# Performance work log

Measured on AMD Instinct MI355X. Metric: run time of the kernel, lower is better.

The kernel has to match this reference:

```python
import jax, jax.numpy as jnp
import numpy as np

B, S, E, D, L, H = 8, 1024, 512, 1024, 8, 16
HD = D // H                 # 64
ROT = max(HD // 2, 32)      # 32
FF = 4 * D
FUSED = 3 * D + 2 * FF      # q,k,v,ff,ff_gate
EPS = 1e-5


def layer_norm(x, w, b):
    mu = jnp.mean(x, axis=-1, keepdims=True)
    var = jnp.mean(jnp.square(x - mu), axis=-1, keepdims=True)
    return (x - mu) * jax.lax.rsqrt(var + EPS) * w + b


def gelu(x):  # fused_gelu from source (erf form, constant 1.41421)
    return x * 0.5 * (1.0 + jax.scipy.special.erf(x / 1.41421))


def silu(x):
    return x * jax.nn.sigmoid(x)


def rotate_half(x):
    x1, x2 = jnp.split(x, 2, axis=-1)
    return jnp.concatenate([-x2, x1], axis=-1)


def rope_tables(seq_len):
    inv = 1.0 / (10000.0 ** (jnp.arange(0, ROT, 2, dtype=jnp.float32) / ROT))
    freqs = jnp.arange(seq_len, dtype=jnp.float32)[:, None] * inv[None, :]
    emb = jnp.concatenate([freqs, freqs], axis=-1)  # [S, ROT]
    # source caches sin/cos in bfloat16 (precision=torch.bfloat16)
    sin = jnp.sin(emb).astype(jnp.bfloat16).astype(jnp.float32)[None, None]
    cos = jnp.cos(emb).astype(jnp.bfloat16).astype(jnp.float32)[None, None]
    return sin, cos  # [1,1,S,ROT]


def setup_inputs() -> dict:
    key = jax.random.key(0)
    ks = jax.random.split(key, 24)
    std = 0.02
    inp = {
        "noisy_embeds": jax.random.normal(ks[0], (B, S, E), jnp.float32),
        "cond_embeds": jax.random.normal(ks[1], (B, S, E), jnp.float32),
        "prev_embeds": jax.random.normal(ks[2], (B, S, E), jnp.float32),
        "infill_mask": jax.random.uniform(ks[3], (B, S, 1), jnp.float32),
        "attention_mask": jnp.zeros((B, 1, 1, S), jnp.float32),
        "times": jax.random.uniform(ks[4], (B,), jnp.float32),
        # time embedding params
        "fourier_w": jax.random.normal(ks[5], (D // 2, 1), jnp.float32),
        "t1_w": jax.random.normal(ks[6], (D, D), jnp.float32) * std,
        "t1_b": jnp.zeros((D,), jnp.float32),
        "t2_w": jax.random.normal(ks[7], (D, D), jnp.float32) * std,
        "t2_b": jnp.zeros((D,), jnp.float32),
        # input projection
        "in_w": jax.random.normal(ks[8], (D, 4 * E), jnp.float32) * std,
        "in_b": jnp.zeros((D,), jnp.float32),
        # per-layer (stacked) block params
        "ln_w": jnp.ones((L, D), jnp.float32),
        "ln_b": jnp.zeros((L, D), jnp.float32),
        "cond_w": jax.random.normal(ks[9], (L, 2 * D, D), jnp.float32) * std,
        "cond_b": jnp.zeros((L, 2 * D), jnp.float32),
        "proj_w": jax.random.normal(ks[10], (L, FUSED, D), jnp.float32) * std,
        "attn_w": jax.random.normal(ks[11], (L, D, D), jnp.float32) * std,
        "attn_b": jnp.zeros((L, D), jnp.float32),
        "ff_w": jax.random.normal(ks[12], (L, D, FF), jnp.float32) * std,
        "ff_b": jnp.zeros((L, D), jnp.float32),
        # output head
        "outln_w": jnp.ones((D,), jnp.float32),
        "outln_b": jnp.zeros((D,), jnp.float32),
        "out_w": jax.random.normal(ks[13], (E, D), jnp.float32) * std,
        "out_b": jnp.zeros((E,), jnp.float32),
        "fin_w": jnp.ones((E,), jnp.float32),
        "fin_b": jnp.zeros((E,), jnp.float32),
    }
    return inp


def _split_heads(x):  # [B,S,H*hd] -> [B,H,S,hd]
    return x.reshape(B, S, H, HD).transpose(0, 2, 1, 3)


def _forward(noisy_embeds, cond_embeds, prev_embeds, infill_mask, attention_mask,
             times, fourier_w, t1_w, t1_b, t2_w, t2_b, in_w, in_b,
             ln_w, ln_b, cond_w, cond_b, proj_w, attn_w, attn_b, ff_w, ff_b,
             outln_w, outln_b, out_w, out_b, fin_w, fin_b):
    # -- time embedding (Random Fourier + MLP) --
    f = 2.0 * np.pi * (times[:, None] @ fourier_w.T)          # [B, D/2]
    te = jnp.concatenate([jnp.cos(f), jnp.sin(f)], axis=-1)   # [B, D]
    te = gelu(te @ t1_w.T + t1_b) @ t2_w.T + t2_b             # [B, D]
    time_embeds = te[:, None, :]                              # [B, 1, D]

    # -- input projection: cat(noisy, cond, prev, mask broadcast) --
    mask_feat = infill_mask * jnp.ones_like(noisy_embeds)     # [B,S,E]
    x = jnp.concatenate([noisy_embeds, cond_embeds, prev_embeds, mask_feat], axis=-1)
    h = x @ in_w.T + in_b                                     # [B,S,D]

    sin, cos = rope_tables(S)
    sm_scale = HD ** (-0.5)

    for i in range(L):
        units = layer_norm(h, ln_w[i], ln_b[i])
        # FiLM conditioning
        sb = silu(time_embeds) @ cond_w[i].T + cond_b[i]      # [B,1,2D]
        scale, bias = jnp.split(sb, 2, axis=-1)
        units = (1.0 + scale) * units + bias
        # fused projection and split
        proj = units @ proj_w[i].T                            # [B,S,11D]
        q, k, v, ff, ff_gate = jnp.split(
            proj, np.cumsum([D, D, D, FF])[:4].tolist(), axis=-1)
        q, k, v = _split_heads(q), _split_heads(k), _split_heads(v)  # [B,H,S,hd]
        # rotary on first ROT dims
        q = jnp.concatenate(
            [q[..., :ROT] * cos + rotate_half(q[..., :ROT]) * sin, q[..., ROT:]], axis=-1)
        k = jnp.concatenate(
            [k[..., :ROT] * cos + rotate_half(k[..., :ROT]) * sin, k[..., ROT:]], axis=-1)
        # NOTE: source scales BOTH q and k by hd^-0.5 (effective hd^-1)
        score = jnp.einsum('bhsd,bhSd->bhsS', q * sm_scale, k * sm_scale)
        score = score + attention_mask
        w = jax.nn.softmax(score, axis=-1)
        attn = jnp.einsum('bhsS,bhSd->bhsd', w, v)
        merged = attn.transpose(0, 2, 1, 3).reshape(B, S, D)
        attn_out = merged @ attn_w[i].T + attn_b[i]
        ff_out = (ff * gelu(ff_gate)) @ ff_w[i].T + ff_b[i]
        h = h + attn_out + ff_out

    out = layer_norm(h, outln_w, outln_b) @ out_w.T + out_b   # [B,S,E]
    return layer_norm(out, fin_w, fin_b)


def reference(noisy_embeds, cond_embeds, prev_embeds, infill_mask, attention_mask,
              times, fourier_w, t1_w, t1_b, t2_w, t2_b, in_w, in_b,
              ln_w, ln_b, cond_w, cond_b, proj_w, attn_w, attn_b, ff_w, ff_b,
              outln_w, outln_b, out_w, out_b, fin_w, fin_b):
    return _forward(noisy_embeds, cond_embeds, prev_embeds, infill_mask, attention_mask,
                    times, fourier_w, t1_w, t1_b, t2_w, t2_b, in_w, in_b,
                    ln_w, ln_b, cond_w, cond_b, proj_w, attn_w, attn_b, ff_w, ff_b,
                    outln_w, outln_b, out_w, out_b, fin_w, fin_b)
```

## Files before the change

kernel.cpp:

```cpp
#include <hip/hip_runtime.h>
#include <hip/hip_bf16.h>
#include <cstddef>
#include <cstdint>

#define BB 8
#define SS 1024
#define EE 512
#define DD 1024
#define LL 8
#define HH 16
#define HD 64
#define ROT 32
#define FF 4096
#define FUSED 11264
#define NTOK 8192
#define QKVW 3072

using u16 = unsigned short;
typedef __attribute__((ext_vector_type(8))) __bf16 bf16x8;
typedef __attribute__((ext_vector_type(4))) float f32x4;
typedef __attribute__((ext_vector_type(4))) unsigned short u16x4;
typedef __attribute__((ext_vector_type(8))) unsigned short u16x8;

typedef const __attribute__((address_space(1))) void gas_t;
typedef __attribute__((address_space(3))) void las_t;

__device__ __forceinline__ void gld16(const void* g, void* l) {
  __builtin_amdgcn_global_load_lds((gas_t*)g, (las_t*)l, 16, 0, 0);
}

__device__ __forceinline__ float bf2f(u16 u) {
  union { unsigned int i; float f; } v; v.i = ((unsigned int)u) << 16; return v.f;
}
__device__ __forceinline__ u16 f2bf(float f) {
  union { float f; unsigned int i; } v; v.f = f;
  unsigned int u = v.i;
  unsigned int r = u + 0x7FFFu + ((u >> 16) & 1u);
  return (u16)(r >> 16);
}
__device__ __forceinline__ float gelu_f(float x) {
  return x * 0.5f * (1.0f + erff(x / 1.41421f));
}
__device__ __forceinline__ float silu_f(float x) {
  return x / (1.0f + __expf(-x));
}

template <int ACCUM, int OUTBF16>
__global__ __launch_bounds__(256, 2) void gemm_bt(
    const u16* __restrict__ A, const u16* __restrict__ W,
    const float* __restrict__ bias, void* __restrict__ Cp,
    int M, int N, int K) {
  __shared__ __align__(16) u16 As[2][128 * 64];
  __shared__ __align__(16) u16 Bs[2][128 * 64];
  const int tid = threadIdx.x;
  const int w = tid >> 6, lane = tid & 63;
  const int m0 = blockIdx.y * 128, n0 = blockIdx.x * 128;
  const int wm = w >> 1, wn = w & 1;

  f32x4 acc[4][4] = {};

  auto stage = [&](int buf, int k0) {
#pragma unroll
    for (int i = 0; i < 4; i++) {
      const int c = w + i * 4;
      const int r = c * 8 + (lane >> 3);
      const int colb = ((lane & 7) << 4) ^ ((r & 7) << 4);
      gld16(A + (size_t)(m0 + r) * K + k0 + (colb >> 1), &As[buf][c * 512]);
      gld16(W + (size_t)(n0 + r) * K + k0 + (colb >> 1), &Bs[buf][c * 512]);
    }
  };

  const int nt = K >> 6;
  stage(0, 0);
  stage(1, 64);
  __syncthreads();

  for (int t = 0; t < nt; t++) {
    const int cur = t & 1;
    bf16x8 av0[4], bv0[4], av1[4], bv1[4];
#pragma unroll
    for (int m = 0; m < 4; m++) {
      const int row = wm * 64 + m * 16 + (lane & 15);
      const int sw = (row & 7) << 4;
      av0[m] = *(const bf16x8*)((const char*)As[cur] + row * 128 + ((((lane >> 4) << 4)) ^ sw));
      av1[m] = *(const bf16x8*)((const char*)As[cur] + row * 128 + ((64 + ((lane >> 4) << 4)) ^ sw));
    }
#pragma unroll
    for (int n = 0; n < 4; n++) {
      const int row = wn * 64 + n * 16 + (lane & 15);
      const int sw = (row & 7) << 4;
      bv0[n] = *(const bf16x8*)((const char*)Bs[cur] + row * 128 + ((((lane >> 4) << 4)) ^ sw));
      bv1[n] = *(const bf16x8*)((const char*)Bs[cur] + row * 128 + ((64 + ((lane >> 4) << 4)) ^ sw));
    }
    __builtin_amdgcn_s_setprio(1);
#pragma unroll
    for (int m = 0; m < 4; m++)
#pragma unroll
      for (int n = 0; n < 4; n++)
        acc[m][n] = __builtin_amdgcn_mfma_f32_16x16x32_bf16(av0[m], bv0[n], acc[m][n], 0, 0, 0);
    __builtin_amdgcn_s_setprio(0);
    __builtin_amdgcn_sched_barrier(0);
    __syncthreads();
    if (t + 2 < nt) stage(cur, (t + 2) << 6);
    __builtin_amdgcn_s_setprio(1);
#pragma unroll
    for (int m = 0; m < 4; m++)
#pragma unroll
      for (int n = 0; n < 4; n++)
        acc[m][n] = __builtin_amdgcn_mfma_f32_16x16x32_bf16(av1[m], bv1[n], acc[m][n], 0, 0, 0);
    __builtin_amdgcn_s_setprio(0);
  }

  const int rowb0 = m0 + wm * 64 + ((lane >> 4) << 2);
  const int colb0 = n0 + wn * 64 + (lane & 15);
#pragma unroll
  for (int n = 0; n < 4; n++) {
    const int col = colb0 + n * 16;
    const float bn = bias ? bias[col] : 0.0f;
#pragma unroll
    for (int m = 0; m < 4; m++) {
#pragma unroll
      for (int r = 0; r < 4; r++) {
        const size_t idx = (size_t)(rowb0 + m * 16 + r) * N + col;
        const float v = acc[m][n][r] + bn;
        if (ACCUM) {
          ((float*)Cp)[idx] += v;
        } else if (OUTBF16) {
          ((u16*)Cp)[idx] = f2bf(v);
        } else {
          ((float*)Cp)[idx] = v;
        }
      }
    }
  }
}

template <int GATED>
__global__ __launch_bounds__(512, 2) void gemm_bt256(
    const u16* __restrict__ A, const u16* __restrict__ W,
    void* __restrict__ Cp, int M, int N, int K) {
  __shared__ __align__(16) u16 As[2][256 * 64];
  __shared__ __align__(16) u16 Bs[2][256 * 64];
  const int tid = threadIdx.x;
  const int w = tid >> 6, lane = tid & 63;
  const int m0 = blockIdx.y * 256, n0 = blockIdx.x * 256;
  const int wm = w >> 2, wn = w & 3;

  f32x4 acc[8][4] = {};

  auto stage = [&](int buf, int k0) {
#pragma unroll
    for (int i = 0; i < 4; i++) {
      const int c = w + i * 8;
      const int r = c * 8 + (lane >> 3);
      const int colb = ((lane & 7) << 4) ^ ((r & 7) << 4);
      gld16(A + (size_t)(m0 + r) * K + k0 + (colb >> 1), &As[buf][c * 512]);
      gld16(W + (size_t)(n0 + r) * K + k0 + (colb >> 1), &Bs[buf][c * 512]);
    }
  };

  const int nt = K >> 6;
  stage(0, 0);
  stage(1, 64);
  __syncthreads();

  for (int t = 0; t < nt; t++) {
    const int cur = t & 1;
    {
      bf16x8 av0[8], bv0[4];
#pragma unroll
      for (int m = 0; m < 8; m++) {
        const int row = wm * 128 + m * 16 + (lane & 15);
        const int cb = (((lane >> 4) << 4)) ^ ((row & 7) << 4);
        av0[m] = *(const bf16x8*)((const char*)As[cur] + row * 128 + cb);
      }
#pragma unroll
      for (int n = 0; n < 4; n++) {
        const int row = wn * 64 + n * 16 + (lane & 15);
        const int cb = (((lane >> 4) << 4)) ^ ((row & 7) << 4);
        bv0[n] = *(const bf16x8*)((const char*)Bs[cur] + row * 128 + cb);
      }
      __builtin_amdgcn_s_setprio(1);
#pragma unroll
      for (int m = 0; m < 8; m++)
#pragma unroll
        for (int n = 0; n < 4; n++)
          acc[m][n] = __builtin_amdgcn_mfma_f32_16x16x32_bf16(av0[m], bv0[n], acc[m][n], 0, 0, 0);
      __builtin_amdgcn_s_setprio(0);
    }
    bf16x8 av1[8], bv1[4];
#pragma unroll
    for (int m = 0; m < 8; m++) {
      const int row = wm * 128 + m * 16 + (lane & 15);
      const int cb = (64 + ((lane >> 4) << 4)) ^ ((row & 7) << 4);
      av1[m] = *(const bf16x8*)((const char*)As[cur] + row * 128 + cb);
    }
#pragma unroll
    for (int n = 0; n < 4; n++) {
      const int row = wn * 64 + n * 16 + (lane & 15);
      const int cb = (64 + ((lane >> 4) << 4)) ^ ((row & 7) << 4);
      bv1[n] = *(const bf16x8*)((const char*)Bs[cur] + row * 128 + cb);
    }
    __builtin_amdgcn_sched_barrier(0);
    __syncthreads();
    if (t + 2 < nt) stage(cur, (t + 2) << 6);
    __builtin_amdgcn_s_setprio(1);
#pragma unroll
    for (int m = 0; m < 8; m++)
#pragma unroll
      for (int n = 0; n < 4; n++)
        acc[m][n] = __builtin_amdgcn_mfma_f32_16x16x32_bf16(av1[m], bv1[n], acc[m][n], 0, 0, 0);
    __builtin_amdgcn_s_setprio(0);
  }

  const int rowb0 = m0 + wm * 128 + ((lane >> 4) << 2);
  if (GATED) {
    const int No = N >> 1;
#pragma unroll
    for (int n = 0; n < 4; n += 2) {
      const int outcol = (n0 >> 1) + wn * 32 + ((n >> 1) << 4) + (lane & 15);
#pragma unroll
      for (int m = 0; m < 8; m++)
#pragma unroll
        for (int r = 0; r < 4; r++) {
          const float fv = acc[m][n][r];
          const float gv = acc[m][n + 1][r];
          ((u16*)Cp)[(size_t)(rowb0 + m * 16 + r) * No + outcol] = f2bf(fv * gelu_f(gv));
        }
    }
  } else {
    const int colb0 = n0 + wn * 64 + (lane & 15);
#pragma unroll
    for (int n = 0; n < 4; n++) {
      const int col = colb0 + n * 16;
#pragma unroll
      for (int m = 0; m < 8; m++)
#pragma unroll
        for (int r = 0; r < 4; r++)
          ((u16*)Cp)[(size_t)(rowb0 + m * 16 + r) * N + col] = f2bf(acc[m][n][r]);
    }
  }
}

__global__ __launch_bounds__(256, 2) void attn_fwd(
    const u16* __restrict__ qr, const u16* __restrict__ kr,
    const u16* __restrict__ vt, const float* __restrict__ mask,
    u16* __restrict__ merged) {
  __shared__ __align__(16) u16 Ks[2][128 * 64];
  __shared__ __align__(16) u16 Vs[2][64 * 128];
  __shared__ __align__(16) u16 Ps[4][16 * 128];
  const int tid = threadIdx.x, w = tid >> 6, lane = tid & 63;
  const int g = blockIdx.x;
  const int j = g >> 3;
  const int bh = (g & 7) + ((j >> 4) << 3);
  const int qx = j & 15;
  const int b = bh >> 4;
  const int q0 = qx * 64 + w * 16;
  const u16* Qb = qr + (size_t)bh * SS * HD;
  const u16* Kb = kr + (size_t)bh * SS * HD;
  const u16* Vb = vt + (size_t)bh * HD * SS;
  const float* mb = mask + (size_t)b * SS;

  bf16x8 qf0, qf1;
  {
    const int qrow = q0 + (lane & 15);
    const u16* qp = Qb + (size_t)qrow * HD + ((lane >> 4) << 3);
    qf0 = *(const bf16x8*)qp;
    qf1 = *(const bf16x8*)(qp + 32);
  }

  float mrun[4], srun[4];
  f32x4 acc[4] = {};
#pragma unroll
  for (int r = 0; r < 4; r++) { mrun[r] = -1e30f; srun[r] = 0.0f; }

  u16* pw = &Ps[w][0];

  auto stage = [&](int buf, int kv0) {
#pragma unroll
    for (int i = 0; i < 4; i++) {
      const int c = w + i * 4;
      {
        const int r = c * 8 + (lane >> 3);
        const int colb = ((lane & 7) << 4) ^ ((r & 7) << 4);
        gld16(Kb + (size_t)(kv0 + r) * HD + (colb >> 1), &Ks[buf][c * 512]);
      }
      {
        const int d = c * 4 + (lane >> 4);
        const int colb = ((lane & 15) << 4) ^ ((d & 7) << 4);
        gld16(Vb + (size_t)d * SS + kv0 + (colb >> 1), &Vs[buf][c * 512]);
      }
    }
  };

  stage(0, 0);
  __syncthreads();

  for (int t = 0; t < 8; t++) {
    const int cur = t & 1;
    const int kv0 = t * 128;
    if (t < 7) stage(cur ^ 1, kv0 + 128);

    f32x4 p[8];
    __builtin_amdgcn_s_setprio(1);
#pragma unroll
    for (int blk = 0; blk < 8; blk++) {
      const int row = blk * 16 + (lane & 15);
      const int swz = (row & 7) << 4;
      const bf16x8 k0v = *(const bf16x8*)((const char*)Ks[cur] + row * 128 + ((((lane >> 4) << 4)) ^ swz));
      const bf16x8 k1v = *(const bf16x8*)((const char*)Ks[cur] + row * 128 + ((64 + ((lane >> 4) << 4)) ^ swz));
      f32x4 z = {};
      p[blk] = __builtin_amdgcn_mfma_f32_16x16x32_bf16(qf0, k0v, z, 0, 0, 0);
      p[blk] = __builtin_amdgcn_mfma_f32_16x16x32_bf16(qf1, k1v, p[blk], 0, 0, 0);
    }
    __builtin_amdgcn_s_setprio(0);

    float mv[8];
#pragma unroll
    for (int blk = 0; blk < 8; blk++) mv[blk] = mb[kv0 + blk * 16 + (lane & 15)];
#pragma unroll
    for (int blk = 0; blk < 8; blk++)
#pragma unroll
      for (int r = 0; r < 4; r++) p[blk][r] = p[blk][r] * (1.0f / 64.0f) + mv[blk];

    float fac[4];
#pragma unroll
    for (int r = 0; r < 4; r++) {
      float tm = p[0][r];
#pragma unroll
      for (int blk = 1; blk < 8; blk++) tm = fmaxf(tm, p[blk][r]);
      tm = fmaxf(tm, __shfl_xor(tm, 1));
      tm = fmaxf(tm, __shfl_xor(tm, 2));
      tm = fmaxf(tm, __shfl_xor(tm, 4));
      tm = fmaxf(tm, __shfl_xor(tm, 8));
      const float mn = fmaxf(mrun[r], tm);
      fac[r] = __expf(mrun[r] - mn);
      mrun[r] = mn;
      float rs = 0.0f;
#pragma unroll
      for (int blk = 0; blk < 8; blk++) {
        const float e = __expf(p[blk][r] - mn);
        p[blk][r] = e;
        rs += e;
      }
      rs += __shfl_xor(rs, 1);
      rs += __shfl_xor(rs, 2);
      rs += __shfl_xor(rs, 4);
      rs += __shfl_xor(rs, 8);
      srun[r] = srun[r] * fac[r] + rs;
    }
#pragma unroll
    for (int dblk = 0; dblk < 4; dblk++)
#pragma unroll
      for (int r = 0; r < 4; r++) acc[dblk][r] *= fac[r];

#pragma unroll
    for (int blk = 0; blk < 8; blk++)
#pragma unroll
      for (int r = 0; r < 4; r++) {
        const int q = ((lane >> 4) << 2) + r;
        pw[(q * 128 + blk * 16 + (lane & 15)) ^ ((q & 7) << 3)] = f2bf(p[blk][r]);
      }

    bf16x8 pa[4];
#pragma unroll
    for (int ks = 0; ks < 4; ks++) {
      const int q = lane & 15;
      pa[ks] = *(const bf16x8*)(pw + ((q * 128 + ks * 32 + ((lane >> 4) << 3)) ^ ((q & 7) << 3)));
    }

    __builtin_amdgcn_s_setprio(1);
#pragma unroll
    for (int dblk = 0; dblk < 4; dblk++) {
      const int drow = dblk * 16 + (lane & 15);
      const int swz = (drow & 7) << 4;
#pragma unroll
      for (int ks = 0; ks < 4; ks++) {
        const bf16x8 vv = *(const bf16x8*)((const char*)Vs[cur] + drow * 256 + ((ks * 64 + ((lane >> 4) << 4)) ^ swz));
        acc[dblk] = __builtin_amdgcn_mfma_f32_16x16x32_bf16(pa[ks], vv, acc[dblk], 0, 0, 0);
      }
    }
    __builtin_amdgcn_s_setprio(0);

    __syncthreads();
  }

#pragma unroll
  for (int dblk = 0; dblk < 4; dblk++)
#pragma unroll
    for (int r = 0; r < 4; r++) {
      const int sq = q0 + ((lane >> 4) << 2) + r;
      const int d = dblk * 16 + (lane & 15);
      merged[((size_t)b * SS + sq) * DD + (bh & 15) * HD + d] = f2bf(acc[dblk][r] / srun[r]);
    }
}

__global__ __launch_bounds__(256) void ln_mod(
    const float* __restrict__ x, const float* __restrict__ lw,
    const float* __restrict__ lb, const float* __restrict__ sb,
    u16* __restrict__ out) {
  const int row = blockIdx.x, tid = threadIdx.x;
  const float4 v = ((const float4*)(x + (size_t)row * DD))[tid];
  float vv[4] = {v.x, v.y, v.z, v.w};
  float s = vv[0] + vv[1] + vv[2] + vv[3];
  float q = vv[0] * vv[0] + vv[1] * vv[1] + vv[2] * vv[2] + vv[3] * vv[3];
  for (int off = 1; off < 64; off <<= 1) {
    s += __shfl_xor(s, off);
    q += __shfl_xor(q, off);
  }
  __shared__ float red[8];
  const int w = tid >> 6, lane = tid & 63;
  if (lane == 0) { red[w] = s; red[4 + w] = q; }
  __syncthreads();
  s = red[0] + red[1] + red[2] + red[3];
  q = red[4] + red[5] + red[6] + red[7];
  const float mu = s * (1.0f / DD);
  const float inv = rsqrtf(q * (1.0f / DD) - mu * mu + 1e-5f);
  const int b = row >> 10;
  u16x4 o;
#pragma unroll
  for (int j = 0; j < 4; j++) {
    const int d = tid * 4 + j;
    float g = (vv[j] - mu) * inv * lw[d] + lb[d];
    if (sb) g = (1.0f + sb[(size_t)b * 2048 + d]) * g + sb[(size_t)b * 2048 + DD + d];
    o[j] = f2bf(g);
  }
  *(u16x4*)(out + (size_t)row * DD + tid * 4) = o;
}

__global__ __launch_bounds__(128) void ln_fin(
    const float* __restrict__ x, const float* __restrict__ w_,
    const float* __restrict__ b_, float* __restrict__ out) {
  const int row = blockIdx.x, tid = threadIdx.x;
  const float4 v = ((const float4*)(x + (size_t)row * EE))[tid];
  float vv[4] = {v.x, v.y, v.z, v.w};
  float s = vv[0] + vv[1] + vv[2] + vv[3];
  float q = vv[0] * vv[0] + vv[1] * vv[1] + vv[2] * vv[2] + vv[3] * vv[3];
  for (int off = 1; off < 64; off <<= 1) {
    s += __shfl_xor(s, off);
    q += __shfl_xor(q, off);
  }
  __shared__ float red[4];
  const int w = tid >> 6, lane = tid & 63;
  if (lane == 0) { red[w] = s; red[2 + w] = q; }
  __syncthreads();
  s = red[0] + red[1];
  q = red[2] + red[3];
  const float mu = s * (1.0f / EE);
  const float inv = rsqrtf(q * (1.0f / EE) - mu * mu + 1e-5f);
  float4 o;
  o.x = (vv[0] - mu) * inv * w_[tid * 4 + 0] + b_[tid * 4 + 0];
  o.y = (vv[1] - mu) * inv * w_[tid * 4 + 1] + b_[tid * 4 + 1];
  o.z = (vv[2] - mu) * inv * w_[tid * 4 + 2] + b_[tid * 4 + 2];
  o.w = (vv[3] - mu) * inv * w_[tid * 4 + 3] + b_[tid * 4 + 3];
  ((float4*)(out + (size_t)row * EE))[tid] = o;
}

template <int IA, int OA>
__global__ __launch_bounds__(256) void vec_gemm(
    const float* __restrict__ in, const float* __restrict__ W,
    const float* __restrict__ bias, float* __restrict__ out, int N, int K) {
  const int n = blockIdx.x * 256 + threadIdx.x;
  const int b = blockIdx.y, l = blockIdx.z;
  const float* ir = in + (size_t)b * K;
  const float* wr = W + ((size_t)l * N + n) * K;
  float s = bias[(size_t)l * N + n];
  for (int k = 0; k < K; k += 4) {
    float4 a = *(const float4*)(ir + k);
    const float4 ww = *(const float4*)(wr + k);
    if (IA) { a.x = silu_f(a.x); a.y = silu_f(a.y); a.z = silu_f(a.z); a.w = silu_f(a.w); }
    s += a.x * ww.x + a.y * ww.y + a.z * ww.z + a.w * ww.w;
  }
  if (OA) s = gelu_f(s);
  out[((size_t)l * gridDim.y + b) * N + n] = s;
}

__global__ void time_fourier(const float* __restrict__ times,
                             const float* __restrict__ fw, float* __restrict__ te0) {
  const int j = blockIdx.x * 256 + threadIdx.x;
  const int b = blockIdx.y;
  const float f = 6.28318530717958647692f * times[b] * fw[j];
  te0[(size_t)b * DD + j] = cosf(f);
  te0[(size_t)b * DD + 512 + j] = sinf(f);
}

__global__ void rope_tab(float* __restrict__ st, float* __restrict__ ct) {
  const int s = blockIdx.x;
  const int j = threadIdx.x;
  const int i = j & 15;
  const float inv = powf(10000.0f, -(float)i * (1.0f / 16.0f));
  const float f = (float)s * inv;
  st[s * 32 + j] = bf2f(f2bf(sinf(f)));
  ct[s * 32 + j] = bf2f(f2bf(cosf(f)));
}

__global__ void build_x(const float* __restrict__ a, const float* __restrict__ b,
                        const float* __restrict__ c, const float* __restrict__ m,
                        u16* __restrict__ x) {
  const size_t i4 = ((size_t)blockIdx.x * 256 + threadIdx.x) * 4;
  if (i4 >= (size_t)NTOK * 2048) return;
  const size_t tok = i4 >> 11;
  const int e = (int)(i4 & 2047);
  float4 v;
  if (e < 512)       v = *(const float4*)(a + tok * 512 + e);
  else if (e < 1024) v = *(const float4*)(b + tok * 512 + (e - 512));
  else if (e < 1536) v = *(const float4*)(c + tok * 512 + (e - 1024));
  else { const float mm = m[tok]; v = make_float4(mm, mm, mm, mm); }
  u16x4 o;
  o[0] = f2bf(v.x); o[1] = f2bf(v.y); o[2] = f2bf(v.z); o[3] = f2bf(v.w);
  *(u16x4*)(x + i4) = o;
}

__global__ void rope_qk(const u16* __restrict__ proj, const float* __restrict__ st,
                        const float* __restrict__ ct, u16* __restrict__ q,
                        u16* __restrict__ k) {
  const size_t idx = (size_t)blockIdx.x * 256 + threadIdx.x;
  const size_t tok = idx >> 10;
  const int hd = (int)(idx & 1023);
  const int hh = hd >> 6, d = hd & 63;
  const int s = (int)(tok & 1023);
  const size_t bb = tok >> 10;
  const u16* pr = proj + tok * QKVW;
  float qv = bf2f(pr[hd]);
  float kv = bf2f(pr[DD + hd]);
  if (d < ROT) {
    const float cs = ct[s * 32 + d], sn = st[s * 32 + d];
    const int pidx = hd - d + ((d < 16) ? d + 16 : d - 16);
    const float qp = bf2f(pr[pidx]);
    const float kp = bf2f(pr[DD + pidx]);
    const float sg = (d < 16) ? -1.0f : 1.0f;
    qv = qv * cs + sg * qp * sn;
    kv = kv * cs + sg * kp * sn;
  }
  const size_t o = ((bb * HH + hh) * SS + s) * HD + d;
  q[o] = f2bf(qv);
  k[o] = f2bf(kv);
}

__global__ __launch_bounds__(256) void transp_v(const u16* __restrict__ proj,
                                                u16* __restrict__ v) {
  __shared__ u16 tile[64 * 72];
  const int tid = threadIdx.x;
  const int s0 = blockIdx.x * 64, h = blockIdx.y, b = blockIdx.z;
  {
    const int sl = tid >> 2, qd = (tid & 3) * 16;
    const u16* src = proj + (size_t)(b * SS + s0 + sl) * QKVW + 2 * DD + h * 64 + qd;
    const u16x8 a0 = *(const u16x8*)src;
    const u16x8 a1 = *(const u16x8*)(src + 8);
    *(u16x8*)&tile[sl * 72 + qd] = a0;
    *(u16x8*)&tile[sl * 72 + qd + 8] = a1;
  }
  __syncthreads();
  {
    const int dl = tid >> 2, qs = (tid & 3) * 16;
    u16x8 o0, o1;
#pragma unroll
    for (int j = 0; j < 8; j++) o0[j] = tile[(qs + j) * 72 + dl];
#pragma unroll
    for (int j = 0; j < 8; j++) o1[j] = tile[(qs + 8 + j) * 72 + dl];
    u16* dst = v + ((size_t)(b * HH + h) * HD + dl) * SS + s0 + qs;
    *(u16x8*)dst = o0;
    *(u16x8*)(dst + 8) = o1;
  }
}

__global__ void cast_bf16(const float* __restrict__ in, u16* __restrict__ out, size_t n4) {
  const size_t i = (size_t)blockIdx.x * 256 + threadIdx.x;
  if (i >= n4) return;
  const float4 v = ((const float4*)in)[i];
  u16x4 o;
  o[0] = f2bf(v.x); o[1] = f2bf(v.y); o[2] = f2bf(v.z); o[3] = f2bf(v.w);
  ((u16x4*)out)[i] = o;
}

__global__ void cast_q(const float* __restrict__ src, u16* __restrict__ dst) {
  const int i = blockIdx.x * 256 + threadIdx.x;
  const int l = blockIdx.y;
  const int r = i >> 7, cb = (i & 127) * 8;
  const float* s = src + ((size_t)l * FUSED + r) * DD + cb;
  const float4 a = *(const float4*)s;
  const float4 b = *(const float4*)(s + 4);
  u16x8 o;
  o[0] = f2bf(a.x); o[1] = f2bf(a.y); o[2] = f2bf(a.z); o[3] = f2bf(a.w);
  o[4] = f2bf(b.x); o[5] = f2bf(b.y); o[6] = f2bf(b.z); o[7] = f2bf(b.w);
  *(u16x8*)(dst + ((size_t)l * QKVW + r) * DD + cb) = o;
}

__global__ void cast_ffg(const float* __restrict__ src, u16* __restrict__ dst) {
  const int i = blockIdx.x * 256 + threadIdx.x;
  const int l = blockIdx.y;
  const int r = i >> 7, cb = (i & 127) * 8;
  const int t16 = r >> 4, pos = r & 15;
  const int j = (t16 >> 1) * 16 + pos;
  const int srow = (t16 & 1) ? (3 * DD + FF + j) : (3 * DD + j);
  const float* s = src + ((size_t)l * FUSED + srow) * DD + cb;
  const float4 a = *(const float4*)s;
  const float4 b = *(const float4*)(s + 4);
  u16x8 o;
  o[0] = f2bf(a.x); o[1] = f2bf(a.y); o[2] = f2bf(a.z); o[3] = f2bf(a.w);
  o[4] = f2bf(b.x); o[5] = f2bf(b.y); o[6] = f2bf(b.z); o[7] = f2bf(b.w);
  *(u16x8*)(dst + ((size_t)l * 8192 + r) * DD + cb) = o;
}

extern "C" void kernel_launch(void* const* d_in, const int* in_sizes, int n_in,
                              void* d_out, int out_size, void* d_ws, size_t ws_size,
                              hipStream_t stream) {
  const float* noisy   = (const float*)d_in[0];
  const float* condi   = (const float*)d_in[1];
  const float* prev    = (const float*)d_in[2];
  const float* infill  = (const float*)d_in[3];
  const float* amask   = (const float*)d_in[4];
  const float* times   = (const float*)d_in[5];
  const float* fourier = (const float*)d_in[6];
  const float* t1_w    = (const float*)d_in[7];
  const float* t1_b    = (const float*)d_in[8];
  const float* t2_w    = (const float*)d_in[9];
  const float* t2_b    = (const float*)d_in[10];
  const float* in_w    = (const float*)d_in[11];
  const float* in_b    = (const float*)d_in[12];
  const float* ln_w    = (const float*)d_in[13];
  const float* ln_b    = (const float*)d_in[14];
  const float* cond_w  = (const float*)d_in[15];
  const float* cond_b  = (const float*)d_in[16];
  const float* proj_w  = (const float*)d_in[17];
  const float* attn_w  = (const float*)d_in[18];
  const float* attn_b  = (const float*)d_in[19];
  const float* ff_w    = (const float*)d_in[20];
  const float* ff_b    = (const float*)d_in[21];
  const float* outln_w = (const float*)d_in[22];
  const float* outln_b = (const float*)d_in[23];
  const float* out_w   = (const float*)d_in[24];
  const float* out_b   = (const float*)d_in[25];
  const float* fin_w   = (const float*)d_in[26];
  const float* fin_b   = (const float*)d_in[27];
  float* outp = (float*)d_out;

  char* p = (char*)d_ws;
  auto alloc = [&](size_t bytes) -> char* {
    char* r = p;
    p += (bytes + 255) & ~(size_t)255;
    return r;
  };
  u16* in_w_h   = (u16*)alloc((size_t)DD * 2048 * 2);
  u16* projq_w_h = (u16*)alloc((size_t)LL * QKVW * DD * 2);
  u16* ffg_w_h  = (u16*)alloc((size_t)LL * 8192 * DD * 2);
  u16* attn_w_h = (u16*)alloc((size_t)LL * DD * DD * 2);
  u16* ff_w_h   = (u16*)alloc((size_t)LL * DD * FF * 2);
  u16* out_w_h  = (u16*)alloc((size_t)EE * DD * 2);
  float* te0 = (float*)alloc((size_t)BB * DD * 4);
  float* te1 = (float*)alloc((size_t)BB * DD * 4);
  float* te2 = (float*)alloc((size_t)BB * DD * 4);
  float* sb  = (float*)alloc((size_t)LL * BB * 2048 * 4);
  float* stab = (float*)alloc((size_t)SS * 32 * 4);
  float* ctab = (float*)alloc((size_t)SS * 32 * 4);
  u16* xb    = (u16*)alloc((size_t)NTOK * 2048 * 2);
  float* h   = (float*)alloc((size_t)NTOK * DD * 4);
  u16* units = (u16*)alloc((size_t)NTOK * DD * 2);
  u16* projq = (u16*)alloc((size_t)NTOK * QKVW * 2);
  u16* qrb   = (u16*)alloc((size_t)NTOK * DD * 2);
  u16* krb   = (u16*)alloc((size_t)NTOK * DD * 2);
  u16* vtb   = (u16*)alloc((size_t)NTOK * DD * 2);
  u16* mg    = (u16*)alloc((size_t)NTOK * DD * 2);
  u16* ffa   = (u16*)alloc((size_t)NTOK * FF * 2);
  u16* hn    = (u16*)alloc((size_t)NTOK * DD * 2);
  float* ob  = (float*)alloc((size_t)NTOK * EE * 4);

  auto castN = [&](const float* src, u16* dst, size_t n) {
    const size_t n4 = n / 4;
    cast_bf16<<<dim3((unsigned)((n4 + 255) / 256)), dim3(256), 0, stream>>>(src, dst, n4);
  };
  castN(in_w, in_w_h, (size_t)DD * 2048);
  cast_q<<<dim3(QKVW * 128 / 256, LL), 256, 0, stream>>>(proj_w, projq_w_h);
  cast_ffg<<<dim3(8192 * 128 / 256, LL), 256, 0, stream>>>(proj_w, ffg_w_h);
  castN(attn_w, attn_w_h, (size_t)LL * DD * DD);
  castN(ff_w, ff_w_h, (size_t)LL * DD * FF);
  castN(out_w, out_w_h, (size_t)EE * DD);

  time_fourier<<<dim3(2, BB), 256, 0, stream>>>(times, fourier, te0);
  vec_gemm<0, 1><<<dim3(4, BB, 1), 256, 0, stream>>>(te0, t1_w, t1_b, te1, 1024, 1024);
  vec_gemm<0, 0><<<dim3(4, BB, 1), 256, 0, stream>>>(te1, t2_w, t2_b, te2, 1024, 1024);
  vec_gemm<1, 0><<<dim3(8, BB, LL), 256, 0, stream>>>(te2, cond_w, cond_b, sb, 2048, 1024);
  rope_tab<<<SS, 32, 0, stream>>>(stab, ctab);
  build_x<<<16384, 256, 0, stream>>>(noisy, condi, prev, infill, xb);
  gemm_bt<0, 0><<<dim3(DD / 128, NTOK / 128), 256, 0, stream>>>(xb, in_w_h, in_b, h, NTOK, DD, 2048);

  for (int l = 0; l < LL; l++) {
    ln_mod<<<NTOK, 256, 0, stream>>>(h, ln_w + (size_t)l * DD, ln_b + (size_t)l * DD,
                                     sb + (size_t)l * BB * 2048, units);
    gemm_bt<0, 1><<<dim3(QKVW / 128, NTOK / 128), 256, 0, stream>>>(
        units, projq_w_h + (size_t)l * QKVW * DD, nullptr, projq, NTOK, QKVW, DD);
    gemm_bt256<1><<<dim3(8192 / 256, NTOK / 256), 512, 0, stream>>>(
        units, ffg_w_h + (size_t)l * 8192 * DD, ffa, NTOK, 8192, DD);
    rope_qk<<<32768, 256, 0, stream>>>(projq, stab, ctab, qrb, krb);
    transp_v<<<dim3(SS / 64, HH, BB), 256, 0, stream>>>(projq, vtb);
    attn_fwd<<<dim3(2048), 256, 0, stream>>>(qrb, krb, vtb, amask, mg);
    gemm_bt<1, 0><<<dim3(DD / 128, NTOK / 128), 256, 0, stream>>>(
        mg, attn_w_h + (size_t)l * DD * DD, attn_b + (size_t)l * DD, h, NTOK, DD, DD);
    gemm_bt<1, 0><<<dim3(DD / 128, NTOK / 128), 256, 0, stream>>>(
        ffa, ff_w_h + (size_t)l * DD * FF, ff_b + (size_t)l * DD, h, NTOK, DD, FF);
  }

  ln_mod<<<NTOK, 256, 0, stream>>>(h, outln_w, outln_b, nullptr, hn);
  gemm_bt<0, 0><<<dim3(EE / 128, NTOK / 128), 256, 0, stream>>>(hn, out_w_h, out_b, ob, NTOK, EE, DD);
  ln_fin<<<NTOK, 128, 0, stream>>>(ob, fin_w, fin_b, outp);
}
```

Measured before the change: 4.882 ms.

## Fuse attention-out and FF-out GEMMs via concatenated K; restructure GEMM prefetch pipeline

The attention output and the gated FF activations are written side by side into one buffer, and the attn_w and ff_w weights are concatenated along K. The two accumulating GEMMs per layer become one GEMM with K=5120 and a pre-summed bias, which removes one read-modify-write of the fp32 residual and one launch per layer. Both GEMM kernels also change their double-buffer schedule: the next tile is issued at the top of each iteration, guarded by a vmcnt wait and raw s_barriers, replacing the mid-iteration __syncthreads prefetch. This shortens prefetch distance to one tile and relies on manual waitcnt correctness.

```diff
diff --git a/kernel.cpp b/kernel.cpp
--- a/kernel.cpp
+++ b/kernel.cpp
@@ -15,6 +15,7 @@
 #define FUSED 11264
 #define NTOK 8192
 #define QKVW 3072
+#define CATW 5120
 
 using u16 = unsigned short;
 typedef __attribute__((ext_vector_type(8))) __bf16 bf16x8;
@@ -24,6 +25,9 @@
 
 typedef const __attribute__((address_space(1))) void gas_t;
 typedef __attribute__((address_space(3))) void las_t;
+
+#define VMCNT8 asm volatile("s_waitcnt vmcnt(8)" ::: "memory")
+#define VMCNT0 asm volatile("s_waitcnt vmcnt(0)" ::: "memory")
 
 __device__ __forceinline__ void gld16(const void* g, void* l) {
   __builtin_amdgcn_global_load_lds((gas_t*)g, (las_t*)l, 16, 0, 0);
@@ -72,11 +76,17 @@
 
   const int nt = K >> 6;
   stage(0, 0);
-  stage(1, 64);
-  __syncthreads();
 
   for (int t = 0; t < nt; t++) {
     const int cur = t & 1;
+    if (t + 1 < nt) {
+      stage(cur ^ 1, (t + 1) << 6);
+      VMCNT8;
+    } else {
+      VMCNT0;
+    }
+    __builtin_amdgcn_s_barrier();
+
     bf16x8 av0[4], bv0[4], av1[4], bv1[4];
 #pragma unroll
     for (int m = 0; m < 4; m++) {
@@ -98,17 +108,13 @@
 #pragma unroll
       for (int n = 0; n < 4; n++)
         acc[m][n] = __builtin_amdgcn_mfma_f32_16x16x32_bf16(av0[m], bv0[n], acc[m][n], 0, 0, 0);
-    __builtin_amdgcn_s_setprio(0);
-    __builtin_amdgcn_sched_barrier(0);
-    __syncthreads();
-    if (t + 2 < nt) stage(cur, (t + 2) << 6);
-    __builtin_amdgcn_s_setprio(1);
 #pragma unroll
     for (int m = 0; m < 4; m++)
 #pragma unroll
       for (int n = 0; n < 4; n++)
         acc[m][n] = __builtin_amdgcn_mfma_f32_16x16x32_bf16(av1[m], bv1[n], acc[m][n], 0, 0, 0);
     __builtin_amdgcn_s_setprio(0);
+    __builtin_amdgcn_s_barrier();
   }
 
   const int rowb0 = m0 + wm * 64 + ((lane >> 4) << 2);
@@ -138,7 +144,7 @@
 template <int GATED>
 __global__ __launch_bounds__(512, 2) void gemm_bt256(
     const u16* __restrict__ A, const u16* __restrict__ W,
-    void* __restrict__ Cp, int M, int N, int K) {
+    void* __restrict__ Cp, int M, int N, int K, int ostride, int ocol0) {
   __shared__ __align__(16) u16 As[2][256 * 64];
   __shared__ __align__(16) u16 Bs[2][256 * 64];
   const int tid = threadIdx.x;
@@ -161,11 +167,17 @@
 
   const int nt = K >> 6;
   stage(0, 0);
-  stage(1, 64);
-  __syncthreads();
 
   for (int t = 0; t < nt; t++) {
     const int cur = t & 1;
+    if (t + 1 < nt) {
+      stage(cur ^ 1, (t + 1) << 6);
+      VMCNT8;
+    } else {
+      VMCNT0;
+    }
+    __builtin_amdgcn_s_barrier();
+
     {
       bf16x8 av0[8], bv0[4];
 #pragma unroll
@@ -188,34 +200,33 @@
           acc[m][n] = __builtin_amdgcn_mfma_f32_16x16x32_bf16(av0[m], bv0[n], acc[m][n], 0, 0, 0);
       __builtin_amdgcn_s_setprio(0);
     }
-    bf16x8 av1[8], bv1[4];
-#pragma unroll
-    for (int m = 0; m < 8; m++) {
-      const int row = wm * 128 + m * 16 + (lane & 15);
-      const int cb = (64 + ((lane >> 4) << 4)) ^ ((row & 7) << 4);
-      av1[m] = *(const bf16x8*)((const char*)As[cur] + row * 128 + cb);
-    }
-#pragma unroll
-    for (int n = 0; n < 4; n++) {
-      const int row = wn * 64 + n * 16 + (lane & 15);
-      const int cb = (64 + ((lane >> 4) << 4)) ^ ((row & 7) << 4);
-      bv1[n] = *(const bf16x8*)((const char*)Bs[cur] + row * 128 + cb);
-    }
-    __builtin_amdgcn_sched_barrier(0);
-    __syncthreads();
-    if (t + 2 < nt) stage(cur, (t + 2) << 6);
-    __builtin_amdgcn_s_setprio(1);
-#pragma unroll
-    for (int m = 0; m < 8; m++)
-#pragma unroll
-      for (int n = 0; n < 4; n++)
-        acc[m][n] = __builtin_amdgcn_mfma_f32_16x16x32_bf16(av1[m], bv1[n], acc[m][n], 0, 0, 0);
-    __builtin_amdgcn_s_setprio(0);
+    {
+      bf16x8 av1[8], bv1[4];
+#pragma unroll
+      for (int m = 0; m < 8; m++) {
+        const int row = wm * 128 + m * 16 + (lane & 15);
+        const int cb = (64 + ((lane >> 4) << 4)) ^ ((row & 7) << 4);
+        av1[m] = *(const bf16x8*)((const char*)As[cur] + row * 128 + cb);
+      }
+#pragma unroll
+      for (int n = 0; n < 4; n++) {
+        const int row = wn * 64 + n * 16 + (lane & 15);
+        const int cb = (64 + ((lane >> 4) << 4)) ^ ((row & 7) << 4);
+        bv1[n] = *(const bf16x8*)((const char*)Bs[cur] + row * 128 + cb);
+      }
+      __builtin_amdgcn_s_setprio(1);
+#pragma unroll
+      for (int m = 0; m < 8; m++)
+#pragma unroll
+        for (int n = 0; n < 4; n++)
+          acc[m][n] = __builtin_amdgcn_mfma_f32_16x16x32_bf16(av1[m], bv1[n], acc[m][n], 0, 0, 0);
+      __builtin_amdgcn_s_setprio(0);
+    }
+    __builtin_amdgcn_s_barrier();
   }
 
   const int rowb0 = m0 + wm * 128 + ((lane >> 4) << 2);
   if (GATED) {
-    const int No = N >> 1;
 #pragma unroll
     for (int n = 0; n < 4; n += 2) {
       const int outcol = (n0 >> 1) + wn * 32 + ((n >> 1) << 4) + (lane & 15);
@@ -225,7 +236,8 @@
         for (int r = 0; r < 4; r++) {
           const float fv = acc[m][n][r];
           const float gv = acc[m][n + 1][r];
-          ((u16*)Cp)[(size_t)(rowb0 + m * 16 + r) * No + outcol] = f2bf(fv * gelu_f(gv));
+          ((u16*)Cp)[(size_t)(rowb0 + m * 16 + r) * ostride + ocol0 + outcol] =
+              f2bf(fv * gelu_f(gv));
         }
     }
   } else {
@@ -245,7 +257,7 @@
 __global__ __launch_bounds__(256, 2) void attn_fwd(
     const u16* __restrict__ qr, const u16* __restrict__ kr,
     const u16* __restrict__ vt, const float* __restrict__ mask,
-    u16* __restrict__ merged) {
+    u16* __restrict__ acat) {
   __shared__ __align__(16) u16 Ks[2][128 * 64];
   __shared__ __align__(16) u16 Vs[2][64 * 128];
   __shared__ __align__(16) u16 Ps[4][16 * 128];
@@ -391,7 +403,7 @@
     for (int r = 0; r < 4; r++) {
       const int sq = q0 + ((lane >> 4) << 2) + r;
       const int d = dblk * 16 + (lane & 15);
-      merged[((size_t)b * SS + sq) * DD + (bh & 15) * HD + d] = f2bf(acc[dblk][r] / srun[r]);
+      acat[((size_t)b * SS + sq) * CATW + (bh & 15) * HD + d] = f2bf(acc[dblk][r] / srun[r]);
     }
 }
 
@@ -600,6 +612,27 @@
   o[0] = f2bf(a.x); o[1] = f2bf(a.y); o[2] = f2bf(a.z); o[3] = f2bf(a.w);
   o[4] = f2bf(b.x); o[5] = f2bf(b.y); o[6] = f2bf(b.z); o[7] = f2bf(b.w);
   *(u16x8*)(dst + ((size_t)l * 8192 + r) * DD + cb) = o;
+}
+
+__global__ void cast_catw(const float* __restrict__ aw, const float* __restrict__ fw,
+                          u16* __restrict__ dst) {
+  const int i = blockIdx.x * 256 + threadIdx.x;
+  const int l = blockIdx.y;
+  const int n = i / 640, cb = (i % 640) * 8;
+  const float* s = (cb < DD) ? (aw + ((size_t)l * DD + n) * DD + cb)
+                             : (fw + ((size_t)l * DD + n) * FF + (cb - DD));
+  const float4 a = *(const float4*)s;
+  const float4 b = *(const float4*)(s + 4);
+  u16x8 o;
+  o[0] = f2bf(a.x); o[1] = f2bf(a.y); o[2] = f2bf(a.z); o[3] = f2bf(a.w);
+  o[4] = f2bf(b.x); o[5] = f2bf(b.y); o[6] = f2bf(b.z); o[7] = f2bf(b.w);
+  *(u16x8*)(dst + ((size_t)l * DD + n) * CATW + cb) = o;
+}
+
+__global__ void add_bias(const float* __restrict__ a, const float* __restrict__ b,
+                         float* __restrict__ o, int n) {
+  const int i = blockIdx.x * 256 + threadIdx.x;
+  if (i < n) o[i] = a[i] + b[i];
 }
 
 extern "C" void kernel_launch(void* const* d_in, const int* in_sizes, int n_in,
@@ -641,12 +674,12 @@
     p += (bytes + 255) & ~(size_t)255;
     return r;
   };
-  u16* in_w_h   = (u16*)alloc((size_t)DD * 2048 * 2);
+  u16* in_w_h    = (u16*)alloc((size_t)DD * 2048 * 2);
   u16* projq_w_h = (u16*)alloc((size_t)LL * QKVW * DD * 2);
-  u16* ffg_w_h  = (u16*)alloc((size_t)LL * 8192 * DD * 2);
-  u16* attn_w_h = (u16*)alloc((size_t)LL * DD * DD * 2);
-  u16* ff_w_h   = (u16*)alloc((size_t)LL * DD * FF * 2);
-  u16* out_w_h  = (u16*)alloc((size_t)EE * DD * 2);
+  u16* ffg_w_h   = (u16*)alloc((size_t)LL * 8192 * DD * 2);
+  u16* cat_w_h   = (u16*)alloc((size_t)LL * DD * CATW * 2);
+  float* cat_b   = (float*)alloc((size_t)LL * DD * 4);
+  u16* out_w_h   = (u16*)alloc((size_t)EE * DD * 2);
   float* te0 = (float*)alloc((size_t)BB * DD * 4);
   float* te1 = (float*)alloc((size_t)BB * DD * 4);
   float* te2 = (float*)alloc((size_t)BB * DD * 4);
@@ -660,8 +693,7 @@
   u16* qrb   = (u16*)alloc((size_t)NTOK * DD * 2);
   u16* krb   = (u16*)alloc((size_t)NTOK * DD * 2);
   u16* vtb   = (u16*)alloc((size_t)NTOK * DD * 2);
-  u16* mg    = (u16*)alloc((size_t)NTOK * DD * 2);
-  u16* ffa   = (u16*)alloc((size_t)NTOK * FF * 2);
+  u16* acat  = (u16*)alloc((size_t)NTOK * CATW * 2);
   u16* hn    = (u16*)alloc((size_t)NTOK * DD * 2);
   float* ob  = (float*)alloc((size_t)NTOK * EE * 4);
 
@@ -672,8 +704,8 @@
   castN(in_w, in_w_h, (size_t)DD * 2048);
   cast_q<<<dim3(QKVW * 128 / 256, LL), 256, 0, stream>>>(proj_w, projq_w_h);
   cast_ffg<<<dim3(8192 * 128 / 256, LL), 256, 0, stream>>>(proj_w, ffg_w_h);
-  castN(attn_w, attn_w_h, (size_t)LL * DD * DD);
-  castN(ff_w, ff_w_h, (size_t)LL * DD * FF);
+  cast_catw<<<dim3(DD * 640 / 256, LL), 256, 0, stream>>>(attn_w, ff_w, cat_w_h);
+  add_bias<<<dim3(LL * DD / 256), 256, 0, stream>>>(attn_b, ff_b, cat_b, LL * DD);
   castN(out_w, out_w_h, (size_t)EE * DD);
 
   time_fourier<<<dim3(2, BB), 256, 0, stream>>>(times, fourier, te0);
@@ -690,14 +722,12 @@
     gemm_bt<0, 1><<<dim3(QKVW / 128, NTOK / 128), 256, 0, stream>>>(
         units, projq_w_h + (size_t)l * QKVW * DD, nullptr, projq, NTOK, QKVW, DD);
     gemm_bt256<1><<<dim3(8192 / 256, NTOK / 256), 512, 0, stream>>>(
-        units, ffg_w_h + (size_t)l * 8192 * DD, ffa, NTOK, 8192, DD);
+        units, ffg_w_h + (size_t)l * 8192 * DD, acat, NTOK, 8192, DD, CATW, DD);
     rope_qk<<<32768, 256, 0, stream>>>(projq, stab, ctab, qrb, krb);
     transp_v<<<dim3(SS / 64, HH, BB), 256, 0, stream>>>(projq, vtb);
-    attn_fwd<<<dim3(2048), 256, 0, stream>>>(qrb, krb, vtb, amask, mg);
+    attn_fwd<<<dim3(2048), 256, 0, stream>>>(qrb, krb, vtb, amask, acat);
     gemm_bt<1, 0><<<dim3(DD / 128, NTOK / 128), 256, 0, stream>>>(
-        mg, attn_w_h + (size_t)l * DD * DD, attn_b + (size_t)l * DD, h, NTOK, DD, DD);
-    gemm_bt<1, 0><<<dim3(DD / 128, NTOK / 128), 256, 0, stream>>>(
-        ffa, ff_w_h + (size_t)l * DD * FF, ff_b + (size_t)l * DD, h, NTOK, DD, FF);
+        acat, cat_w_h + (size_t)l * DD * CATW, cat_b + (size_t)l * DD, h, NTOK, DD, CATW);
   }
 
   ln_mod<<<NTOK, 256, 0, stream>>>(h, outln_w, outln_b, nullptr, hn);
```

New measurement: 4.804 ms. About the same (-1.6%).
